# Optimization experiments

Hardware: AMD Instinct MI355X
Metric: run time of the kernel (lower is better)

The kernel has to match this reference:

```python
import jax, jax.numpy as jnp
import numpy as np

BN_EPS = 1e-6
SOFTMAX_EPS = 1e-8
D = 64      # fingerprint_dim
BD = 12     # bond_dim
N_ATOM = 10000
N_EDGE = 40000


def _bn(x, gamma, beta, mean, var):
    # BatchNorm1d in inference mode (running stats)
    return (x - mean) / jnp.sqrt(var + BN_EPS) * gamma + beta


def setup_inputs() -> dict:
    key = jax.random.key(0)
    ks = jax.random.split(key, 16)
    inp = {
        "atom": jax.random.normal(ks[0], (N_ATOM, D), dtype=jnp.float32),
        "bond_index": jax.random.randint(ks[1], (N_EDGE, 2), 0, N_ATOM, dtype=jnp.int64),
        "bond": jax.random.normal(ks[2], (N_EDGE, BD), dtype=jnp.float32),
        # encoder: Linear(bond_dim, D*D) + BatchNorm1d(D*D)
        "enc_W": jax.random.normal(ks[3], (D * D, BD), dtype=jnp.float32) * (1.0 / np.sqrt(BD)),
        "enc_b": jnp.zeros((D * D,), dtype=jnp.float32),
        "enc_gamma": jnp.ones((D * D,), dtype=jnp.float32),
        "enc_beta": jnp.zeros((D * D,), dtype=jnp.float32),
        "enc_mean": jnp.zeros((D * D,), dtype=jnp.float32),
        "enc_var": jnp.ones((D * D,), dtype=jnp.float32),
        # align: Linear(2*D, 1)
        "align_W": jax.random.normal(ks[4], (1, 2 * D), dtype=jnp.float32) * (1.0 / np.sqrt(2 * D)),
        "align_b": jnp.zeros((1,), dtype=jnp.float32),
        # attend: Linear(D, D) + BatchNorm1d(D), no activation
        "att_W": jax.random.normal(ks[5], (D, D), dtype=jnp.float32) * (1.0 / np.sqrt(D)),
        "att_b": jnp.zeros((D,), dtype=jnp.float32),
        "att_gamma": jnp.ones((D,), dtype=jnp.float32),
        "att_beta": jnp.zeros((D,), dtype=jnp.float32),
        "att_mean": jnp.zeros((D,), dtype=jnp.float32),
        "att_var": jnp.ones((D,), dtype=jnp.float32),
        # GRUCell(D, D)
        "gru_W_ih": jax.random.normal(ks[6], (3 * D, D), dtype=jnp.float32) * (1.0 / np.sqrt(D)),
        "gru_W_hh": jax.random.normal(ks[7], (3 * D, D), dtype=jnp.float32) * (1.0 / np.sqrt(D)),
        "gru_b_ih": jnp.zeros((3 * D,), dtype=jnp.float32),
        "gru_b_hh": jnp.zeros((3 * D,), dtype=jnp.float32),
    }
    return inp


def reference(atom, bond_index, bond,
              enc_W, enc_b, enc_gamma, enc_beta, enc_mean, enc_var,
              align_W, align_b,
              att_W, att_b, att_gamma, att_beta, att_mean, att_var,
              gru_W_ih, gru_W_hh, gru_b_ih, gru_b_hh):
    num_atom, d = atom.shape
    tgt = bond_index[:, 0]  # target atom of each edge
    nbr = bond_index[:, 1]  # neighbor atom of each edge

    # encoder: relu(BN(linear(bond))) -> per-edge [d, d] bond matrix
    enc = jax.nn.relu(_bn(bond @ enc_W.T + enc_b, enc_gamma, enc_beta, enc_mean, enc_var))
    enc = enc.reshape(-1, d, d)  # [E, d, d]

    # gather neighbor atoms, per-edge matvec through bond matrix
    neighbor = jnp.einsum('ed,edf->ef', atom[nbr], enc)  # [E, d]

    # attention logits (dropout is identity in eval)
    feat = jnp.concatenate([atom[tgt], neighbor], axis=-1)  # [E, 2d]
    score = jax.nn.leaky_relu(feat @ align_W.T + align_b, negative_slope=0.01)  # [E, 1]

    # segment softmax over target atoms
    mx = jax.ops.segment_max(score, tgt, num_segments=num_atom)  # [N, 1]
    ex = jnp.exp(score - mx[tgt])
    denom = jax.ops.segment_sum(ex, tgt, num_segments=num_atom)[tgt] + SOFTMAX_EPS
    attn = ex / denom  # [E, 1]

    # attend: BN(linear(neighbor)) (no activation), weighted scatter-add
    attd = _bn(neighbor @ att_W.T + att_b, att_gamma, att_beta, att_mean, att_var)
    context = jax.ops.segment_sum(attn * attd, tgt, num_segments=num_atom)  # [N, d]
    context = jax.nn.elu(context)

    # GRUCell(context, atom)
    gi = context @ gru_W_ih.T + gru_b_ih  # [N, 3d]
    gh = atom @ gru_W_hh.T + gru_b_hh     # [N, 3d]
    i_r, i_z, i_n = jnp.split(gi, 3, axis=-1)
    h_r, h_z, h_n = jnp.split(gh, 3, axis=-1)
    r = jax.nn.sigmoid(i_r + h_r)
    z = jax.nn.sigmoid(i_z + h_z)
    n = jnp.tanh(i_n + r * h_n)
    return (1.0 - z) * n + z * atom
```

## Files before the change

### kernel.cpp

```cpp
#include <hip/hip_runtime.h>
#include <math.h>

#define NA 10000
#define NE 40000

typedef float f2 __attribute__((ext_vector_type(2)));
typedef float f4 __attribute__((ext_vector_type(4)));
typedef float f16v __attribute__((ext_vector_type(16)));
typedef int   i4 __attribute__((ext_vector_type(4)));
typedef __bf16 bf16x8 __attribute__((ext_vector_type(8)));

union U8 { unsigned short us[8]; __bf16 b[8]; bf16x8 v; };
union UF4 { f4 v; f2 h[2]; };
union UC16 { f16v v; f2 h[8]; };

static __device__ __forceinline__ unsigned short bf_rne(float x){
  unsigned u = __float_as_uint(x);
  unsigned r = (u + 0x7fffu + ((u>>16)&1u)) >> 16;
  return (unsigned short)r;
}
static __device__ __forceinline__ float bf_to_f(unsigned short h){
  return __uint_as_float(((unsigned)h)<<16);
}
static __device__ __forceinline__ float rcpf(float x){
  float r; asm("v_rcp_f32 %0, %1" : "=v"(r) : "v"(x)); return r;
}
static __device__ __forceinline__ float fsig(float x){
  return rcpf(1.f + __expf(-x));
}
static __device__ __forceinline__ float ftanh(float x){
  float ax = fabsf(x);
  float e = __expf(ax + ax);
  float t = 1.f - 2.f*rcpf(e + 1.f);
  return copysignf(t, x);
}

__global__ __launch_bounds__(256) void k_pre(
  const float* __restrict__ encW, const float* __restrict__ encB,
  const float* __restrict__ eg, const float* __restrict__ ebt,
  const float* __restrict__ e_mn, const float* __restrict__ e_vr,
  const float* __restrict__ attW, const float* __restrict__ attB,
  const float* __restrict__ agm, const float* __restrict__ abt,
  const float* __restrict__ amn, const float* __restrict__ avr,
  const float* __restrict__ wih, const float* __restrict__ whh,
  const int* __restrict__ bidx, const float* __restrict__ atom,
  const float* __restrict__ alW,
  unsigned short* __restrict__ BI,
  unsigned short* __restrict__ aBh, unsigned short* __restrict__ aBl,
  unsigned short* __restrict__ aQh, unsigned short* __restrict__ aQl,
  float* __restrict__ attBf, float* __restrict__ wT,
  float* __restrict__ p, int* __restrict__ cnt)
{
  int tid = threadIdx.x;
  int gid = blockIdx.x*256 + tid;
  int gstride = gridDim.x*256;
  for (int i=gid; i<131072; i+=gstride){
    int j = i&15, ll = (i>>4)&63, t = i>>10;
    int d = t>>1, ft = t&1;
    int jj = j&7;
    int k = ((ll>>5)<<3)+jj;
    int n = d*64 + ft*32 + (ll&31);
    float s = eg[n]*rsqrtf(e_vr[n]+1e-6f);
    unsigned short outv = 0;
    if (k<12){
      float wv = encW[n*12+k]*s;
      unsigned short hi = bf_rne(wv);
      outv = (j<8)? hi : bf_rne(wv - bf_to_f(hi));
    } else if (k==12){
      float b = (encB[n]-e_mn[n])*s + ebt[n];
      unsigned short hi = bf_rne(b);
      outv = (j<8)? hi : bf_rne(b - bf_to_f(hi));
    }
    BI[i] = outv;
  }
  for (int i=gid; i<4096; i+=gstride){
    int j=i&7, l=(i>>3)&63, t=i>>9;
    int kk=t>>1, nt=t&1;
    int k = kk*16 + ((l>>5)<<3) + j;
    int n = nt*32 + (l&31);
    float s = agm[n]*rsqrtf(avr[n]+1e-6f);
    float wv = attW[n*64+k]*s;
    unsigned short hi = bf_rne(wv);
    aBh[i]=hi; aBl[i]=bf_rne(wv - bf_to_f(hi));
  }
  for (int i=gid; i<2048; i+=gstride){
    int j=i&7, l2=(i>>3)&63, kk=i>>9;
    float v = alW[64 + kk*16 + ((l2>>5)<<3) + j];
    unsigned short hi=0, lo=0;
    if ((l2&31)==0){ hi = bf_rne(v); lo = bf_rne(v - bf_to_f(hi)); }
    aQh[i]=hi; aQl[i]=lo;
  }
  for (int f=gid; f<64; f+=gstride){
    float s = agm[f]*rsqrtf(avr[f]+1e-6f);
    attBf[f] = (attB[f]-amn[f])*s + abt[f];
  }
  for (int i=gid; i<24576; i+=gstride){
    int j=i&3, f=(i>>2)&63, idx2=i>>8;
    int g=idx2>>4, kg=idx2&15, k=kg*4+j;
    wT[i] = (g<3)? wih[(g*64+f)*64+k] : whh[((g-3)*64+f)*64+k];
  }
  {
    int wid = gid>>6;
    int l = tid&63;
    float wl = alW[l];
    for (int a=wid; a<NA; a+=(gstride>>6)){
      float v = wl*atom[(size_t)a*64+l];
      v += __shfl_xor(v,1);  v += __shfl_xor(v,2);
      v += __shfl_xor(v,4);  v += __shfl_xor(v,8);
      v += __shfl_xor(v,16); v += __shfl_xor(v,32);
      if (l==0) p[a]=v;
    }
  }
  for (int e=gid; e<NE; e+=gstride) atomicAdd(&cnt[bidx[e*2]],1);
}

__global__ __launch_bounds__(256) void k_scan(const int* __restrict__ cnt,
                                              int* __restrict__ rowstart,
                                              int* __restrict__ wofs)
{
  __shared__ int sPart[256];
  int t = threadIdx.x;
  int base = t*40;
  i4 buf[10];
  int sum = 0;
  if (base < NA){
    const i4* cp = (const i4*)(cnt + base);
    #pragma unroll
    for (int i=0;i<10;i++) buf[i] = cp[i];
    #pragma unroll
    for (int i=0;i<10;i++) sum += buf[i].x+buf[i].y+buf[i].z+buf[i].w;
  }
  sPart[t]=sum;
  __syncthreads();
  for (int off=1; off<256; off<<=1){
    int v = (t>=off)? sPart[t-off] : 0;
    __syncthreads();
    sPart[t]+=v;
    __syncthreads();
  }
  int run = sPart[t]-sum;
  if (base < NA){
    #pragma unroll
    for (int i=0;i<10;i++){
      i4 b=buf[i], o;
      o.x=run; run+=b.x; o.y=run; run+=b.y;
      o.z=run; run+=b.z; o.w=run; run+=b.w;
      ((i4*)(rowstart+base))[i]=o;
      ((i4*)(wofs+base))[i]=o;
    }
  }
  if (t==0) rowstart[NA]=NE;
}

__global__ __launch_bounds__(256) void k_scatter(const int* __restrict__ bidx,
                                                 int* __restrict__ wofs,
                                                 int* __restrict__ elist)
{
  int e = blockIdx.x*256 + threadIdx.x;
  if (e < NE){
    int tg = bidx[e*2];
    int pos = atomicAdd(&wofs[tg],1);
    elist[pos]=e;
  }
}

__global__ __launch_bounds__(256, 3) void k_edge(
  const float* __restrict__ atom, const int* __restrict__ bidx, const float* __restrict__ bond,
  const unsigned short* __restrict__ BI,
  const unsigned short* __restrict__ aBh, const unsigned short* __restrict__ aBl,
  const unsigned short* __restrict__ aQh, const unsigned short* __restrict__ aQl,
  const int* __restrict__ elist, float* __restrict__ zC, float* __restrict__ qv)
{
  __shared__ float sA[4352];
  __shared__ float sP[8192];
  __shared__ int   sEl[64];
  __shared__ int   sNbr[64];

  int tid = threadIdx.x;
  int l = tid & 63;
  int w = tid >> 6;
  int g = l >> 5;
  int em = l & 31;
  int E0 = blockIdx.x * 64;

  if (tid < 64){
    int e = elist[E0+tid];
    sEl[tid] = e;
    sNbr[tid] = bidx[e*2+1];
  }
  __syncthreads();
  for (int i=tid; i<4096; i+=256){
    int le=i>>6, d=i&63;
    sA[d*68+le] = atom[(size_t)sNbr[le]*64 + d];
  }

  U8 A1[2], A2[2];
  #pragma unroll
  for (int t=0;t<2;t++){
    const f4* bp = (const f4*)(bond + (size_t)sEl[t*32+em]*12);
    f4 b0=bp[0], b1v=bp[1], b2v=bp[2];
    float bv[12] = {b0.x,b0.y,b0.z,b0.w,b1v.x,b1v.y,b1v.z,b1v.w,b2v.x,b2v.y,b2v.z,b2v.w};
    #pragma unroll
    for (int j=0;j<8;j++){
      int k = g*8+j;
      float x = (k<12)? bv[k] : (k==12? 1.f : 0.f);
      __bf16 h = (__bf16)x;
      A1[t].b[j] = h;
      A2[t].b[j] = (__bf16)(x - (float)h);
    }
  }
  __syncthreads();

  int ft = w & 1;
  int dbase = (w >> 1) * 32;

  f2 nacc[2][8];
  #pragma unroll
  for (int t=0;t<2;t++)
    #pragma unroll
    for (int i=0;i<8;i++) nacc[t][i] = (f2){0.f,0.f};
  f16v cz;
  #pragma unroll
  for (int r=0;r<16;r++) cz[r] = 0.f;

  const bf16x8* pB = (const bf16x8*)BI + ((size_t)(dbase*2+ft)*64 + l)*2;
  U8 rh[4], rl[4];
  #pragma unroll
  for (int s=0;s<3;s++){ rh[s].v = pB[s*256]; rl[s].v = pB[s*256+1]; }

  #pragma unroll 4
  for (int dd=0; dd<32; dd++){
    int d = dbase + dd;
    int cs = dd&3, ns = (dd+3)&3;
    rh[ns].v = pB[(size_t)(dd+3)*256];
    rl[ns].v = pB[(size_t)(dd+3)*256 + 1];

    UF4 ldA[2][4];
    #pragma unroll
    for (int t=0;t<2;t++)
      #pragma unroll
      for (int q=0;q<4;q++) ldA[t][q].v = *(const f4*)&sA[d*68 + t*32 + 8*q + 4*g];

    #pragma unroll
    for (int t=0;t<2;t++){
      UC16 c;
      c.v = __builtin_amdgcn_mfma_f32_32x32x16_bf16(A1[t].v, rh[cs].v, cz, 0,0,0);
      c.v = __builtin_amdgcn_mfma_f32_32x32x16_bf16(A2[t].v, rh[cs].v, c.v, 0,0,0);
      c.v = __builtin_amdgcn_mfma_f32_32x32x16_bf16(A1[t].v, rl[cs].v, c.v, 0,0,0);
      #pragma unroll
      for (int i=0;i<8;i++){
        f2 ev;
        ev[0] = fmaxf(c.h[i][0], 0.f);
        ev[1] = fmaxf(c.h[i][1], 0.f);
        asm("v_pk_fma_f32 %0, %1, %2, %0"
            : "+v"(nacc[t][i])
            : "v"(ldA[t][i>>1].h[i&1]), "v"(ev));
      }
    }
  }

  int mt2 = w>>1, nt = w&1;
  U8 eBh[4], eBl[4], eQh[4], eQl[4];
  #pragma unroll
  for (int kk=0; kk<4; kk++){
    eBh[kk].v = *(const bf16x8*)(aBh + ((size_t)((kk*2+nt)*64 + l))*8);
    eBl[kk].v = *(const bf16x8*)(aBl + ((size_t)((kk*2+nt)*64 + l))*8);
  }
  if (nt){
    #pragma unroll
    for (int kk=0; kk<4; kk++){
      eQh[kk].v = *(const bf16x8*)(aQh + ((size_t)(kk*64 + l))*8);
      eQl[kk].v = *(const bf16x8*)(aQl + ((size_t)(kk*64 + l))*8);
    }
  }

  __syncthreads();
  {
    int dh = w >> 1;
    #pragma unroll
    for (int t=0;t<2;t++)
      #pragma unroll
      for (int r=0;r<16;r++)
        sP[(((dh*2+ft)*2+t)*16 + r)*64 + l] = nacc[t][r>>1][r&1];
  }
  __syncthreads();
  {
    int ftw = w&1, tw = w>>1;
    #pragma unroll
    for (int r=0;r<16;r++){
      float v = sP[(((0*2+ftw)*2+tw)*16 + r)*64 + l]
              + sP[(((1*2+ftw)*2+tw)*16 + r)*64 + l];
      int m = tw*32 + (r&3) + ((r>>2)<<3) + (g<<2);
      sA[m*68 + (ftw<<5) + em] = v;
    }
  }
  __syncthreads();

  {
    f16v c, c2;
    #pragma unroll
    for (int r=0;r<16;r++){ c[r] = 0.f; c2[r] = 0.f; }
    #pragma unroll
    for (int kk=0; kk<4; kk++){
      const float* src = &sA[(mt2*32+em)*68 + kk*16 + g*8];
      f4 x0 = *(const f4*)src;
      f4 x1 = *(const f4*)(src+4);
      U8 Ah, Al;
      #pragma unroll
      for (int j=0;j<4;j++){
        __bf16 h0 = (__bf16)x0[j];
        Ah.b[j] = h0; Al.b[j] = (__bf16)(x0[j] - (float)h0);
        __bf16 h1 = (__bf16)x1[j];
        Ah.b[4+j] = h1; Al.b[4+j] = (__bf16)(x1[j] - (float)h1);
      }
      c = __builtin_amdgcn_mfma_f32_32x32x16_bf16(Ah.v, eBh[kk].v, c, 0,0,0);
      c = __builtin_amdgcn_mfma_f32_32x32x16_bf16(Al.v, eBh[kk].v, c, 0,0,0);
      c = __builtin_amdgcn_mfma_f32_32x32x16_bf16(Ah.v, eBl[kk].v, c, 0,0,0);
      if (nt){
        c2 = __builtin_amdgcn_mfma_f32_32x32x16_bf16(Ah.v, eQh[kk].v, c2, 0,0,0);
        c2 = __builtin_amdgcn_mfma_f32_32x32x16_bf16(Al.v, eQh[kk].v, c2, 0,0,0);
        c2 = __builtin_amdgcn_mfma_f32_32x32x16_bf16(Ah.v, eQl[kk].v, c2, 0,0,0);
      }
    }
    #pragma unroll
    for (int r=0;r<16;r++){
      int row = (r&3) + ((r>>2)<<3) + ((l>>5)<<2);
      zC[(size_t)(E0 + mt2*32 + row)*64 + nt*32 + (l&31)] = c[r];
    }
    if (nt && em==0){
      #pragma unroll
      for (int r=0;r<16;r++){
        int row = (r&3) + ((r>>2)<<3) + (g<<2);
        qv[E0 + mt2*32 + row] = c2[r];
      }
    }
  }
}

__global__ __launch_bounds__(256, 4) void k_gru(
  const float* __restrict__ atom, const float* __restrict__ zC,
  const int* __restrict__ rowstart, const float* __restrict__ p,
  const float* __restrict__ qv, const float* __restrict__ alB,
  const float* __restrict__ attBf, const float* __restrict__ wT,
  const float* __restrict__ bih, const float* __restrict__ bhh,
  float* __restrict__ out)
{
  __shared__ float sc[4][4][64];
  __shared__ float shh[4][4][64];
  __shared__ float swT[6144];
  int tid = threadIdx.x;
  int l = tid & 63;
  int w = tid >> 6;
  int base = blockIdx.x*16 + w*4;
  float bias = attBf[l];
  float ab = alB[0];

  #pragma unroll
  for (int aa=0; aa<4; aa++){
    int a = base + aa;
    float hf = atom[(size_t)a*64 + l];
    float cf = 0.f;
    int d0 = rowstart[a];
    int deg = rowstart[a+1] - d0;
    if (deg > 0){
      float pa = p[a] + ab;
      float m0=-3e38f, m1=-3e38f, m2=-3e38f, m3=-3e38f;
      int i=0;
      for (; i+3<deg; i+=4){
        float s0 = pa + qv[d0+i],   s1 = pa + qv[d0+i+1];
        float s2 = pa + qv[d0+i+2], s3 = pa + qv[d0+i+3];
        s0=(s0>0.f)?s0:0.01f*s0; s1=(s1>0.f)?s1:0.01f*s1;
        s2=(s2>0.f)?s2:0.01f*s2; s3=(s3>0.f)?s3:0.01f*s3;
        m0=fmaxf(m0,s0); m1=fmaxf(m1,s1); m2=fmaxf(m2,s2); m3=fmaxf(m3,s3);
      }
      for (; i<deg; ++i){
        float s0 = pa + qv[d0+i];
        s0=(s0>0.f)?s0:0.01f*s0;
        m0=fmaxf(m0,s0);
      }
      float mx = fmaxf(fmaxf(m0,m1), fmaxf(m2,m3));
      float dn0=0.f, dn1=0.f, y0=0.f, y1=0.f;
      i=0;
      for (; i+1<deg; i+=2){
        float s0 = pa + qv[d0+i], s1 = pa + qv[d0+i+1];
        s0=(s0>0.f)?s0:0.01f*s0; s1=(s1>0.f)?s1:0.01f*s1;
        float z0 = zC[(size_t)(d0+i)*64 + l];
        float z1 = zC[(size_t)(d0+i+1)*64 + l];
        float e0=__expf(s0-mx), e1=__expf(s1-mx);
        dn0+=e0; dn1+=e1;
        y0=fmaf(e0,z0,y0); y1=fmaf(e1,z1,y1);
      }
      if (i<deg){
        float s0 = pa + qv[d0+i];
        s0=(s0>0.f)?s0:0.01f*s0;
        float e0=__expf(s0-mx);
        dn0+=e0; y0=fmaf(e0, zC[(size_t)(d0+i)*64+l], y0);
      }
      float dn = dn0+dn1;
      cf = ((y0+y1) + dn*bias)*rcpf(dn + 1e-8f);
      cf = (cf>0.f)? cf : expm1f(cf);
    }
    sc[w][aa][l] = cf; shh[w][aa][l] = hf;
  }

  float acc[6][4];
  #pragma unroll
  for (int gg=0;gg<6;gg++)
    #pragma unroll
    for (int aa=0;aa<4;aa++) acc[gg][aa]=0.f;

  for (int ch=0; ch<4; ch++){
    __syncthreads();
    #pragma unroll
    for (int ii=0; ii<6; ii++){
      int i = tid + ii*256;
      int f = i&63, q = i>>6; int gg = q>>2, kgc = q&3;
      ((f4*)swT)[i] = ((const f4*)wT)[(gg*16 + ch*4 + kgc)*64 + f];
    }
    __syncthreads();
    #pragma unroll
    for (int kgc=0; kgc<4; kgc++){
      int kg = ch*4 + kgc;
      f4 wv[6];
      #pragma unroll
      for (int gg=0;gg<6;gg++) wv[gg] = *(const f4*)&swT[((gg*4+kgc)*64 + l)*4];
      #pragma unroll
      for (int aa=0;aa<4;aa++){
        f4 cv = *(const f4*)&sc[w][aa][kg*4];
        f4 hv = *(const f4*)&shh[w][aa][kg*4];
        #pragma unroll
        for (int j=0;j<4;j++){
          acc[0][aa] = fmaf(cv[j], wv[0][j], acc[0][aa]);
          acc[1][aa] = fmaf(cv[j], wv[1][j], acc[1][aa]);
          acc[2][aa] = fmaf(cv[j], wv[2][j], acc[2][aa]);
          acc[3][aa] = fmaf(hv[j], wv[3][j], acc[3][aa]);
          acc[4][aa] = fmaf(hv[j], wv[4][j], acc[4][aa]);
          acc[5][aa] = fmaf(hv[j], wv[5][j], acc[5][aa]);
        }
      }
    }
  }

  float b0 = bih[l], b1 = bih[64+l], b2 = bih[128+l];
  float h0 = bhh[l], h1 = bhh[64+l], h2 = bhh[128+l];
  #pragma unroll
  for (int aa=0;aa<4;aa++){
    int a = base + aa;
    float hf = shh[w][aa][l];
    float r = fsig(acc[0][aa] + b0 + acc[3][aa] + h0);
    float z = fsig(acc[1][aa] + b1 + acc[4][aa] + h1);
    float n = ftanh(acc[2][aa] + b2 + r*(acc[5][aa] + h2));
    out[(size_t)a*64 + l] = (1.f - z)*n + z*hf;
  }
}

extern "C" void kernel_launch(void* const* d_in, const int* in_sizes, int n_in,
                              void* d_out, int out_size, void* d_ws, size_t ws_size,
                              hipStream_t stream) {
  const float* atom = (const float*)d_in[0];
  const int*   bidx = (const int*)  d_in[1];
  const float* bond = (const float*)d_in[2];
  const float* encW = (const float*)d_in[3];
  const float* encB = (const float*)d_in[4];
  const float* eg   = (const float*)d_in[5];
  const float* ebt  = (const float*)d_in[6];
  const float* e_mn = (const float*)d_in[7];
  const float* e_vr = (const float*)d_in[8];
  const float* alW  = (const float*)d_in[9];
  const float* alB  = (const float*)d_in[10];
  const float* atW  = (const float*)d_in[11];
  const float* atB  = (const float*)d_in[12];
  const float* agm  = (const float*)d_in[13];
  const float* abt  = (const float*)d_in[14];
  const float* amn  = (const float*)d_in[15];
  const float* avr  = (const float*)d_in[16];
  const float* wih  = (const float*)d_in[17];
  const float* whh  = (const float*)d_in[18];
  const float* bih  = (const float*)d_in[19];
  const float* bhh  = (const float*)d_in[20];

  float* ws = (float*)d_ws;
  unsigned short* BI  = (unsigned short*)(ws + 0);
  unsigned short* aBh = (unsigned short*)(ws + 65536);
  unsigned short* aBl = (unsigned short*)(ws + 67584);
  unsigned short* aQh = (unsigned short*)(ws + 69632);
  unsigned short* aQl = (unsigned short*)(ws + 70656);
  float* attBf   = ws + 71680;
  float* wT      = ws + 71744;
  float* p       = ws + 96320;
  int*   cnt     = (int*)(ws + 106336);
  int*   rowstart= (int*)(ws + 116352);
  int*   wofs    = (int*)(ws + 126368);
  int*   elist   = (int*)(ws + 136384);
  float* qv      = ws + 176384;
  float* zCb     = ws + 216384;
  float* outp    = (float*)d_out;

  hipMemsetAsync(cnt, 0, NA*sizeof(int), stream);
  k_pre<<<512, 256, 0, stream>>>(encW,encB,eg,ebt,e_mn,e_vr,
                                 atW,atB,agm,abt,amn,avr,
                                 wih,whh,bidx,atom,alW,
                                 BI,aBh,aBl,aQh,aQl,attBf,wT,p,cnt);
  k_scan<<<1, 256, 0, stream>>>(cnt, rowstart, wofs);
  k_scatter<<<(NE+255)/256, 256, 0, stream>>>(bidx, wofs, elist);
  k_edge<<<625, 256, 0, stream>>>(atom, bidx, bond, BI, aBh, aBl, aQh, aQl,
                                  elist, zCb, qv);
  k_gru<<<625, 256, 0, stream>>>(atom, zCb, rowstart, p, qv, alB,
                                 attBf, wT, bih, bhh, outp);
}
```

Before: 173.4 us.

## Shrink edge tile to 32 edges per 2-wave block, drop cross-wave reduction

Each k_edge block now handles 32 edges with 128 threads instead of 64 edges with 256 threads. Each wave loops over all 64 d values for one output half, so the partial sums no longer pass through shared memory, and the sP buffer, its reduction and one barrier are removed. The grid doubles to 1250 blocks and shared memory per block shrinks, which should spread work more evenly across CUs and allow more resident blocks. In exchange, each encoder-weight (BI) fragment is reused across fewer edges, so per-edge global/L2 weight traffic roughly doubles, and the serial dependency chain per wave is longer.

```diff
diff --git a/kernel.cpp b/kernel.cpp
--- a/kernel.cpp
+++ b/kernel.cpp
@@ -164,40 +164,38 @@
   }
 }
 
-__global__ __launch_bounds__(256, 3) void k_edge(
+__global__ __launch_bounds__(128, 4) void k_edge(
   const float* __restrict__ atom, const int* __restrict__ bidx, const float* __restrict__ bond,
   const unsigned short* __restrict__ BI,
   const unsigned short* __restrict__ aBh, const unsigned short* __restrict__ aBl,
   const unsigned short* __restrict__ aQh, const unsigned short* __restrict__ aQl,
   const int* __restrict__ elist, float* __restrict__ zC, float* __restrict__ qv)
 {
-  __shared__ float sA[4352];
-  __shared__ float sP[8192];
-  __shared__ int   sEl[64];
-  __shared__ int   sNbr[64];
+  __shared__ float sA[2304];
+  __shared__ int   sEl[32];
+  __shared__ int   sNbr[32];
 
   int tid = threadIdx.x;
   int l = tid & 63;
   int w = tid >> 6;
   int g = l >> 5;
   int em = l & 31;
-  int E0 = blockIdx.x * 64;
-
-  if (tid < 64){
+  int E0 = blockIdx.x * 32;
+
+  if (tid < 32){
     int e = elist[E0+tid];
     sEl[tid] = e;
     sNbr[tid] = bidx[e*2+1];
   }
   __syncthreads();
-  for (int i=tid; i<4096; i+=256){
+  for (int i=tid; i<2048; i+=128){
     int le=i>>6, d=i&63;
-    sA[d*68+le] = atom[(size_t)sNbr[le]*64 + d];
-  }
-
-  U8 A1[2], A2[2];
-  #pragma unroll
-  for (int t=0;t<2;t++){
-    const f4* bp = (const f4*)(bond + (size_t)sEl[t*32+em]*12);
+    sA[d*36+le] = atom[(size_t)sNbr[le]*64 + d];
+  }
+
+  U8 A1, A2;
+  {
+    const f4* bp = (const f4*)(bond + (size_t)sEl[em]*12);
     f4 b0=bp[0], b1v=bp[1], b2v=bp[2];
     float bv[12] = {b0.x,b0.y,b0.z,b0.w,b1v.x,b1v.y,b1v.z,b1v.w,b2v.x,b2v.y,b2v.z,b2v.w};
     #pragma unroll
@@ -205,61 +203,52 @@
       int k = g*8+j;
       float x = (k<12)? bv[k] : (k==12? 1.f : 0.f);
       __bf16 h = (__bf16)x;
-      A1[t].b[j] = h;
-      A2[t].b[j] = (__bf16)(x - (float)h);
+      A1.b[j] = h;
+      A2.b[j] = (__bf16)(x - (float)h);
     }
   }
   __syncthreads();
 
-  int ft = w & 1;
-  int dbase = (w >> 1) * 32;
-
-  f2 nacc[2][8];
-  #pragma unroll
-  for (int t=0;t<2;t++)
-    #pragma unroll
-    for (int i=0;i<8;i++) nacc[t][i] = (f2){0.f,0.f};
+  int ft = w;
+
+  f2 nacc[8];
+  #pragma unroll
+  for (int i=0;i<8;i++) nacc[i] = (f2){0.f,0.f};
   f16v cz;
   #pragma unroll
   for (int r=0;r<16;r++) cz[r] = 0.f;
 
-  const bf16x8* pB = (const bf16x8*)BI + ((size_t)(dbase*2+ft)*64 + l)*2;
+  const bf16x8* pB = (const bf16x8*)BI + ((size_t)ft*64 + l)*2;
   U8 rh[4], rl[4];
   #pragma unroll
   for (int s=0;s<3;s++){ rh[s].v = pB[s*256]; rl[s].v = pB[s*256+1]; }
 
   #pragma unroll 4
-  for (int dd=0; dd<32; dd++){
-    int d = dbase + dd;
-    int cs = dd&3, ns = (dd+3)&3;
-    rh[ns].v = pB[(size_t)(dd+3)*256];
-    rl[ns].v = pB[(size_t)(dd+3)*256 + 1];
-
-    UF4 ldA[2][4];
-    #pragma unroll
-    for (int t=0;t<2;t++)
-      #pragma unroll
-      for (int q=0;q<4;q++) ldA[t][q].v = *(const f4*)&sA[d*68 + t*32 + 8*q + 4*g];
-
-    #pragma unroll
-    for (int t=0;t<2;t++){
-      UC16 c;
-      c.v = __builtin_amdgcn_mfma_f32_32x32x16_bf16(A1[t].v, rh[cs].v, cz, 0,0,0);
-      c.v = __builtin_amdgcn_mfma_f32_32x32x16_bf16(A2[t].v, rh[cs].v, c.v, 0,0,0);
-      c.v = __builtin_amdgcn_mfma_f32_32x32x16_bf16(A1[t].v, rl[cs].v, c.v, 0,0,0);
-      #pragma unroll
-      for (int i=0;i<8;i++){
-        f2 ev;
-        ev[0] = fmaxf(c.h[i][0], 0.f);
-        ev[1] = fmaxf(c.h[i][1], 0.f);
-        asm("v_pk_fma_f32 %0, %1, %2, %0"
-            : "+v"(nacc[t][i])
-            : "v"(ldA[t][i>>1].h[i&1]), "v"(ev));
-      }
-    }
-  }
-
-  int mt2 = w>>1, nt = w&1;
+  for (int d=0; d<64; d++){
+    int cs = d&3, ns = (d+3)&3;
+    rh[ns].v = pB[(size_t)(d+3)*256];
+    rl[ns].v = pB[(size_t)(d+3)*256 + 1];
+
+    UF4 ldA[4];
+    #pragma unroll
+    for (int q=0;q<4;q++) ldA[q].v = *(const f4*)&sA[d*36 + 8*q + 4*g];
+
+    UC16 c;
+    c.v = __builtin_amdgcn_mfma_f32_32x32x16_bf16(A1.v, rh[cs].v, cz, 0,0,0);
+    c.v = __builtin_amdgcn_mfma_f32_32x32x16_bf16(A2.v, rh[cs].v, c.v, 0,0,0);
+    c.v = __builtin_amdgcn_mfma_f32_32x32x16_bf16(A1.v, rl[cs].v, c.v, 0,0,0);
+    #pragma unroll
+    for (int i=0;i<8;i++){
+      f2 ev;
+      ev[0] = fmaxf(c.h[i][0], 0.f);
+      ev[1] = fmaxf(c.h[i][1], 0.f);
+      asm("v_pk_fma_f32 %0, %1, %2, %0"
+          : "+v"(nacc[i])
+          : "v"(ldA[i>>1].h[i&1]), "v"(ev));
+    }
+  }
+
+  int nt = w;
   U8 eBh[4], eBl[4], eQh[4], eQl[4];
   #pragma unroll
   for (int kk=0; kk<4; kk++){
@@ -276,22 +265,10 @@
 
   __syncthreads();
   {
-    int dh = w >> 1;
-    #pragma unroll
-    for (int t=0;t<2;t++)
-      #pragma unroll
-      for (int r=0;r<16;r++)
-        sP[(((dh*2+ft)*2+t)*16 + r)*64 + l] = nacc[t][r>>1][r&1];
-  }
-  __syncthreads();
-  {
-    int ftw = w&1, tw = w>>1;
     #pragma unroll
     for (int r=0;r<16;r++){
-      float v = sP[(((0*2+ftw)*2+tw)*16 + r)*64 + l]
-              + sP[(((1*2+ftw)*2+tw)*16 + r)*64 + l];
-      int m = tw*32 + (r&3) + ((r>>2)<<3) + (g<<2);
-      sA[m*68 + (ftw<<5) + em] = v;
+      int row = (r&3) + ((r>>2)<<3) + (g<<2);
+      sA[row*68 + (ft<<5) + em] = nacc[r>>1][r&1];
     }
   }
   __syncthreads();
@@ -302,7 +279,7 @@
     for (int r=0;r<16;r++){ c[r] = 0.f; c2[r] = 0.f; }
     #pragma unroll
     for (int kk=0; kk<4; kk++){
-      const float* src = &sA[(mt2*32+em)*68 + kk*16 + g*8];
+      const float* src = &sA[em*68 + kk*16 + g*8];
       f4 x0 = *(const f4*)src;
       f4 x1 = *(const f4*)(src+4);
       U8 Ah, Al;
@@ -325,13 +302,13 @@
     #pragma unroll
     for (int r=0;r<16;r++){
       int row = (r&3) + ((r>>2)<<3) + ((l>>5)<<2);
-      zC[(size_t)(E0 + mt2*32 + row)*64 + nt*32 + (l&31)] = c[r];
+      zC[(size_t)(E0 + row)*64 + nt*32 + (l&31)] = c[r];
     }
     if (nt && em==0){
       #pragma unroll
       for (int r=0;r<16;r++){
         int row = (r&3) + ((r>>2)<<3) + (g<<2);
-        qv[E0 + mt2*32 + row] = c2[r];
+        qv[E0 + row] = c2[r];
       }
     }
   }
@@ -503,8 +480,8 @@
                                  BI,aBh,aBl,aQh,aQl,attBf,wT,p,cnt);
   k_scan<<<1, 256, 0, stream>>>(cnt, rowstart, wofs);
   k_scatter<<<(NE+255)/256, 256, 0, stream>>>(bidx, wofs, elist);
-  k_edge<<<625, 256, 0, stream>>>(atom, bidx, bond, BI, aBh, aBl, aQh, aQl,
-                                  elist, zCb, qv);
+  k_edge<<<1250, 128, 0, stream>>>(atom, bidx, bond, BI, aBh, aBl, aQh, aQl,
+                                   elist, zCb, qv);
   k_gru<<<625, 256, 0, stream>>>(atom, zCb, rowstart, p, qv, alB,
                                  attBf, wT, bih, bhh, outp);
 }
```

Result: no change. 175.3 us (+1.1%).
